# Kernel tuning notes

Measured on AMD Instinct MI355X. Metric: run time of the kernel, lower is better.

The kernel has to match this reference:

```python
import jax, jax.numpy as jnp
import numpy as np


def setup_inputs() -> dict:
    key = jax.random.key(0)
    ks = jax.random.split(key, 8)
    b, l, d, n = 2, 4096, 1024, 16
    s = 0.02
    return {
        "x": jax.random.normal(ks[0], (b, l, d), dtype=jnp.float32),
        "W1": jax.random.normal(ks[1], (d, d), dtype=jnp.float32) * s,
        "b1": jnp.zeros((d,), dtype=jnp.float32),
        "W2": jax.random.normal(ks[2], (n, d), dtype=jnp.float32) * s,
        "b2": jnp.zeros((n,), dtype=jnp.float32),
        "W3": jax.random.normal(ks[3], (n, d), dtype=jnp.float32) * s,
        "b3": jnp.zeros((n,), dtype=jnp.float32),
        "A": jax.random.normal(ks[4], (d, n), dtype=jnp.float32) * s,
    }


def reference(x, W1, b1, W2, b2, W3, b3, A):
    # Faithful to the torch S6.forward as written:
    #   B = fc2(x); C = fc3(x); delta = softplus(fc1(x))
    #   dB = einsum('bld,bln->bldn', delta, B)
    #   h  = dA * 0 + x[..., None] * dB          (h starts at zeros, no scan)
    #   y  = einsum('bln,bldn->bld', C, h)
    # which collapses exactly to y = x * delta * sum_n(C * B).
    # dA = exp(einsum('bld,dn->bldn', delta, A)) is multiplied by zeros and
    # therefore never influences the output (A is a dead parameter here).
    B = jnp.einsum('bld,nd->bln', x, W2) + b2          # (b, l, n)
    C = jnp.einsum('bld,nd->bln', x, W3) + b3          # (b, l, n)
    delta = jax.nn.softplus(jnp.einsum('bld,ed->ble', x, W1) + b1)  # (b, l, d)
    cb = jnp.sum(C * B, axis=-1)                        # (b, l) = sum_n C*B
    y = x * delta * cb[..., None]                       # (b, l, d)
    return y
```

## Files before the change

### kernel.cpp

```cpp
#include <hip/hip_runtime.h>
#include <hip/hip_bf16.h>
#include <stdint.h>

typedef __attribute__((ext_vector_type(8))) short short8;
typedef __attribute__((ext_vector_type(4))) float f32x4;
typedef __attribute__((ext_vector_type(4))) unsigned short us4;

static __device__ __forceinline__ unsigned short f2bf(float f) {
    __hip_bfloat16 h = __float2bfloat16(f);
    union { __hip_bfloat16 h; unsigned short u; } v; v.h = h;
    return v.u;
}
static __device__ __forceinline__ float bf2f(unsigned short h) {
    union { uint32_t u; float f; } v; v.u = ((uint32_t)h) << 16;
    return v.f;
}

static __device__ __forceinline__ short8 cvt8(float4 a, float4 b) {
    short8 r;
    r[0] = (short)f2bf(a.x); r[1] = (short)f2bf(a.y);
    r[2] = (short)f2bf(a.z); r[3] = (short)f2bf(a.w);
    r[4] = (short)f2bf(b.x); r[5] = (short)f2bf(b.y);
    r[6] = (short)f2bf(b.z); r[7] = (short)f2bf(b.w);
    return r;
}

__global__ __launch_bounds__(256) void cb_fused(
    const float* __restrict__ x,
    const float* __restrict__ W1,
    const float* __restrict__ W2,
    const float* __restrict__ b2,
    const float* __restrict__ W3,
    const float* __restrict__ b3,
    unsigned short* __restrict__ xb,
    unsigned short* __restrict__ w1b,
    float* __restrict__ cbo)
{
    const int bid = blockIdx.x;
    const int t = threadIdx.x;

    if (bid >= 512) {
        const int base = (bid - 512) * 4096 + t;
        const float4* w4 = (const float4*)W1;
#pragma unroll
        for (int i = 0; i < 16; ++i) {
            float4 v = w4[base + i * 256];
            us4 r = { f2bf(v.x), f2bf(v.y), f2bf(v.z), f2bf(v.w) };
            *(us4*)&w1b[(size_t)(base + i * 256) * 4] = r;
        }
        return;
    }

    __shared__ float red[4][2][16][16];

    const int wave = t >> 6, lane = t & 63;
    const int r0 = bid * 16;
    const int rrow = lane & 15;
    const int klane = (lane >> 4) * 8;
    const size_t xrow = (size_t)(r0 + rrow) * 1024;
    const int k0 = wave * 256;

    f32x4 accB = {0.f, 0.f, 0.f, 0.f};
    f32x4 accC = {0.f, 0.f, 0.f, 0.f};

#pragma unroll
    for (int ks = 0; ks < 256; ks += 32) {
        const int k = k0 + ks + klane;
        float4 xa = *(const float4*)&x[xrow + k];
        float4 xc = *(const float4*)&x[xrow + k + 4];
        short8 af = cvt8(xa, xc);
        *(short8*)&xb[xrow + k] = af;
        float4 w2a = *(const float4*)&W2[(size_t)rrow * 1024 + k];
        float4 w2c = *(const float4*)&W2[(size_t)rrow * 1024 + k + 4];
        float4 w3a = *(const float4*)&W3[(size_t)rrow * 1024 + k];
        float4 w3c = *(const float4*)&W3[(size_t)rrow * 1024 + k + 4];
        short8 w2f = cvt8(w2a, w2c);
        short8 w3f = cvt8(w3a, w3c);
        accB = __builtin_amdgcn_mfma_f32_16x16x32_bf16(af, w2f, accB, 0, 0, 0);
        accC = __builtin_amdgcn_mfma_f32_16x16x32_bf16(af, w3f, accC, 0, 0, 0);
    }

#pragma unroll
    for (int j = 0; j < 4; ++j) {
        red[wave][0][(lane >> 4) * 4 + j][lane & 15] = accB[j];
        red[wave][1][(lane >> 4) * 4 + j][lane & 15] = accC[j];
    }
    __syncthreads();

    if (wave == 0) {
        const int n = lane & 15;
        const float b2v = b2[n], b3v = b3[n];
        float prod[4];
#pragma unroll
        for (int j = 0; j < 4; ++j) {
            const int row = (lane >> 4) * 4 + j;
            float Bv = red[0][0][row][n] + red[1][0][row][n]
                     + red[2][0][row][n] + red[3][0][row][n] + b2v;
            float Cv = red[0][1][row][n] + red[1][1][row][n]
                     + red[2][1][row][n] + red[3][1][row][n] + b3v;
            prod[j] = Bv * Cv;
        }
#pragma unroll
        for (int off = 1; off < 16; off <<= 1)
#pragma unroll
            for (int j = 0; j < 4; ++j)
                prod[j] += __shfl_xor(prod[j], off, 64);
        if ((lane & 15) == 0) {
#pragma unroll
            for (int j = 0; j < 4; ++j)
                cbo[r0 + (lane >> 4) * 4 + j] = prod[j];
        }
    }
}

__global__ __launch_bounds__(256, 2) void gemm_kernel(
    const unsigned short* __restrict__ xb,
    const unsigned short* __restrict__ w1b,
    const float* __restrict__ b1,
    const float* __restrict__ cb,
    float* __restrict__ y)
{
    __shared__ unsigned short As[2][128 * 64];
    __shared__ unsigned short Bs[2][128 * 64];

    const int wg = blockIdx.x;
    const int nid = (wg & 7) * 64 + (wg >> 3);
    const int row0 = (nid >> 3) * 128;
    const int col0 = (nid & 7) * 128;

    const int t = threadIdx.x;
    const int wid = t >> 6, lane = t & 63;
    const int wm = wid >> 1, wn = wid & 1;

    const int lrow = lane >> 3;
    const int gslot = (lane & 7) ^ lrow;

    f32x4 acc[4][4];
#pragma unroll
    for (int m = 0; m < 4; ++m)
#pragma unroll
        for (int n = 0; n < 4; ++n)
            acc[m][n] = (f32x4){0.f, 0.f, 0.f, 0.f};

    auto STAGE = [&](int b, int kt) {
#pragma unroll
        for (int p = 0; p < 4; ++p) {
            const int grp = p * 4 + wid;
            const int row = grp * 8 + lrow;
            const int gc = kt + gslot * 8;
            const unsigned short* ga = &xb[(size_t)(row0 + row) * 1024 + gc];
            const unsigned short* gb = &w1b[(size_t)(col0 + row) * 1024 + gc];
            __builtin_amdgcn_global_load_lds(
                (const __attribute__((address_space(1))) void*)ga,
                (__attribute__((address_space(3))) void*)&As[b][grp * 512 + lane * 8], 16, 0, 0);
            __builtin_amdgcn_global_load_lds(
                (const __attribute__((address_space(1))) void*)gb,
                (__attribute__((address_space(3))) void*)&Bs[b][grp * 512 + lane * 8], 16, 0, 0);
        }
    };

    STAGE(0, 0);
    asm volatile("s_waitcnt vmcnt(0)" ::: "memory");
    __builtin_amdgcn_s_barrier();
    __builtin_amdgcn_sched_barrier(0);

    const int ro = lane & 15;
    const int sh = lane >> 4;

    for (int tk = 0; tk < 16; ++tk) {
        const int cur = tk & 1;
        if (tk < 15) {
            STAGE(cur ^ 1, (tk + 1) * 64);
            asm volatile("s_waitcnt vmcnt(8)" ::: "memory");
        } else {
            asm volatile("s_waitcnt vmcnt(0)" ::: "memory");
        }
        __builtin_amdgcn_s_barrier();
        __builtin_amdgcn_sched_barrier(0);

        short8 af[2][4], bfr[2][4];
#pragma unroll
        for (int ks = 0; ks < 2; ++ks) {
            const int s = ks * 4 + sh;
#pragma unroll
            for (int m = 0; m < 4; ++m) {
                const int ar = wm * 64 + m * 16 + ro;
                af[ks][m]  = *(const short8*)&As[cur][ar * 64 + ((s ^ (ro & 7)) << 3)];
                const int br = wn * 64 + m * 16 + ro;
                bfr[ks][m] = *(const short8*)&Bs[cur][br * 64 + ((s ^ (ro & 7)) << 3)];
            }
        }
        __builtin_amdgcn_s_setprio(1);
#pragma unroll
        for (int ks = 0; ks < 2; ++ks)
#pragma unroll
            for (int m = 0; m < 4; ++m)
#pragma unroll
                for (int n = 0; n < 4; ++n)
                    acc[m][n] = __builtin_amdgcn_mfma_f32_16x16x32_bf16(af[ks][m], bfr[ks][n], acc[m][n], 0, 0, 0);
        __builtin_amdgcn_s_setprio(0);

        asm volatile("s_waitcnt lgkmcnt(0)" ::: "memory");
        __builtin_amdgcn_s_barrier();
        __builtin_amdgcn_sched_barrier(0);
    }

#pragma unroll
    for (int m = 0; m < 4; ++m) {
        const int grow_base = row0 + wm * 64 + m * 16 + (lane >> 4) * 4;
#pragma unroll
        for (int n = 0; n < 4; ++n) {
            const int gcol = col0 + wn * 64 + n * 16 + (lane & 15);
            const float bv = b1[gcol];
#pragma unroll
            for (int j = 0; j < 4; ++j) {
                const int grow = grow_base + j;
                const float v = acc[m][n][j] + bv;
                const float sp = (v > 15.f) ? v : __logf(1.f + __expf(v));
                const size_t off = (size_t)grow * 1024 + gcol;
                y[off] = bf2f(xb[off]) * sp * cb[grow];
            }
        }
    }
}

extern "C" void kernel_launch(void* const* d_in, const int* in_sizes, int n_in,
                              void* d_out, int out_size, void* d_ws, size_t ws_size,
                              hipStream_t stream) {
    const float* x  = (const float*)d_in[0];
    const float* W1 = (const float*)d_in[1];
    const float* b1 = (const float*)d_in[2];
    const float* W2 = (const float*)d_in[3];
    const float* b2 = (const float*)d_in[4];
    const float* W3 = (const float*)d_in[5];
    const float* b3 = (const float*)d_in[6];

    float* y = (float*)d_out;

    unsigned short* xb  = (unsigned short*)d_ws;
    unsigned short* w1b = xb + (size_t)8192 * 1024;
    float* cbuf = (float*)(w1b + (size_t)1024 * 1024);

    cb_fused<<<576, 256, 0, stream>>>(x, W1, W2, b2, W3, b3, xb, w1b, cbuf);
    gemm_kernel<<<512, 256, 0, stream>>>(xb, w1b, b1, cbuf, y);
}
```

Before: 46.12 us.

## Split GEMM k-tile staging into halves interleaved with MFMA; widen prologue blocks to 512

The GEMM main loop now issues the next tile's global-to-LDS loads in two halves. The second half is issued between the two k-substeps of MFMA work, and LDS fragment reads are split per substep so loads overlap compute. The first kernel doubles its block size to 512 threads, so each wave covers 128 of K instead of 256 and the reduction runs over 8 waves. This shortens per-wave serial loads in the prologue kernel at the cost of more shared-memory reduction work and a more intricate vmcnt schedule.

```diff
diff --git a/kernel.cpp b/kernel.cpp
--- a/kernel.cpp
+++ b/kernel.cpp
@@ -25,7 +25,7 @@
     return r;
 }
 
-__global__ __launch_bounds__(256) void cb_fused(
+__global__ __launch_bounds__(512) void cb_fused(
     const float* __restrict__ x,
     const float* __restrict__ W1,
     const float* __restrict__ W2,
@@ -43,28 +43,28 @@
         const int base = (bid - 512) * 4096 + t;
         const float4* w4 = (const float4*)W1;
 #pragma unroll
-        for (int i = 0; i < 16; ++i) {
-            float4 v = w4[base + i * 256];
+        for (int i = 0; i < 8; ++i) {
+            float4 v = w4[base + i * 512];
             us4 r = { f2bf(v.x), f2bf(v.y), f2bf(v.z), f2bf(v.w) };
-            *(us4*)&w1b[(size_t)(base + i * 256) * 4] = r;
+            *(us4*)&w1b[(size_t)(base + i * 512) * 4] = r;
         }
         return;
     }
 
-    __shared__ float red[4][2][16][16];
+    __shared__ float red[8][2][16][16];
 
     const int wave = t >> 6, lane = t & 63;
     const int r0 = bid * 16;
     const int rrow = lane & 15;
     const int klane = (lane >> 4) * 8;
     const size_t xrow = (size_t)(r0 + rrow) * 1024;
-    const int k0 = wave * 256;
+    const int k0 = wave * 128;
 
     f32x4 accB = {0.f, 0.f, 0.f, 0.f};
     f32x4 accC = {0.f, 0.f, 0.f, 0.f};
 
 #pragma unroll
-    for (int ks = 0; ks < 256; ks += 32) {
+    for (int ks = 0; ks < 128; ks += 32) {
         const int k = k0 + ks + klane;
         float4 xa = *(const float4*)&x[xrow + k];
         float4 xc = *(const float4*)&x[xrow + k + 4];
@@ -94,10 +94,12 @@
 #pragma unroll
         for (int j = 0; j < 4; ++j) {
             const int row = (lane >> 4) * 4 + j;
-            float Bv = red[0][0][row][n] + red[1][0][row][n]
-                     + red[2][0][row][n] + red[3][0][row][n] + b2v;
-            float Cv = red[0][1][row][n] + red[1][1][row][n]
-                     + red[2][1][row][n] + red[3][1][row][n] + b3v;
+            float Bv = b2v, Cv = b3v;
+#pragma unroll
+            for (int w = 0; w < 8; ++w) {
+                Bv += red[w][0][row][n];
+                Cv += red[w][1][row][n];
+            }
             prod[j] = Bv * Cv;
         }
 #pragma unroll
@@ -142,9 +144,9 @@
         for (int n = 0; n < 4; ++n)
             acc[m][n] = (f32x4){0.f, 0.f, 0.f, 0.f};
 
-    auto STAGE = [&](int b, int kt) {
-#pragma unroll
-        for (int p = 0; p < 4; ++p) {
+    auto STAGE_HALF = [&](int b, int kt, int h) {
+#pragma unroll
+        for (int p = 2 * h; p < 2 * h + 2; ++p) {
             const int grp = p * 4 + wid;
             const int row = grp * 8 + lrow;
             const int gc = kt + gslot * 8;
@@ -159,48 +161,62 @@
         }
     };
 
-    STAGE(0, 0);
-    asm volatile("s_waitcnt vmcnt(0)" ::: "memory");
-    __builtin_amdgcn_s_barrier();
-    __builtin_amdgcn_sched_barrier(0);
+    STAGE_HALF(0, 0, 0);
+    STAGE_HALF(0, 0, 1);
 
     const int ro = lane & 15;
     const int sh = lane >> 4;
 
     for (int tk = 0; tk < 16; ++tk) {
         const int cur = tk & 1;
+
         if (tk < 15) {
-            STAGE(cur ^ 1, (tk + 1) * 64);
-            asm volatile("s_waitcnt vmcnt(8)" ::: "memory");
+            STAGE_HALF(cur ^ 1, (tk + 1) * 64, 0);
+            asm volatile("s_waitcnt vmcnt(4)" ::: "memory");
         } else {
             asm volatile("s_waitcnt vmcnt(0)" ::: "memory");
         }
         __builtin_amdgcn_s_barrier();
         __builtin_amdgcn_sched_barrier(0);
 
-        short8 af[2][4], bfr[2][4];
-#pragma unroll
-        for (int ks = 0; ks < 2; ++ks) {
-            const int s = ks * 4 + sh;
+        short8 af[4], bfr[4];
+        {
+            const int s = (sh ^ (ro & 7)) << 3;
 #pragma unroll
             for (int m = 0; m < 4; ++m) {
-                const int ar = wm * 64 + m * 16 + ro;
-                af[ks][m]  = *(const short8*)&As[cur][ar * 64 + ((s ^ (ro & 7)) << 3)];
-                const int br = wn * 64 + m * 16 + ro;
-                bfr[ks][m] = *(const short8*)&Bs[cur][br * 64 + ((s ^ (ro & 7)) << 3)];
-            }
-        }
+                af[m]  = *(const short8*)&As[cur][(wm * 64 + m * 16 + ro) * 64 + s];
+                bfr[m] = *(const short8*)&Bs[cur][(wn * 64 + m * 16 + ro) * 64 + s];
+            }
+        }
+        asm volatile("s_waitcnt lgkmcnt(0)" ::: "memory");
+        __builtin_amdgcn_sched_barrier(0);
         __builtin_amdgcn_s_setprio(1);
 #pragma unroll
-        for (int ks = 0; ks < 2; ++ks)
-#pragma unroll
-            for (int m = 0; m < 4; ++m)
-#pragma unroll
-                for (int n = 0; n < 4; ++n)
-                    acc[m][n] = __builtin_amdgcn_mfma_f32_16x16x32_bf16(af[ks][m], bfr[ks][n], acc[m][n], 0, 0, 0);
+        for (int m = 0; m < 4; ++m)
+#pragma unroll
+            for (int n = 0; n < 4; ++n)
+                acc[m][n] = __builtin_amdgcn_mfma_f32_16x16x32_bf16(af[m], bfr[n], acc[m][n], 0, 0, 0);
         __builtin_amdgcn_s_setprio(0);
 
+        if (tk < 15) STAGE_HALF(cur ^ 1, (tk + 1) * 64, 1);
+        {
+            const int s = ((4 + sh) ^ (ro & 7)) << 3;
+#pragma unroll
+            for (int m = 0; m < 4; ++m) {
+                af[m]  = *(const short8*)&As[cur][(wm * 64 + m * 16 + ro) * 64 + s];
+                bfr[m] = *(const short8*)&Bs[cur][(wn * 64 + m * 16 + ro) * 64 + s];
+            }
+        }
         asm volatile("s_waitcnt lgkmcnt(0)" ::: "memory");
+        __builtin_amdgcn_sched_barrier(0);
+        __builtin_amdgcn_s_setprio(1);
+#pragma unroll
+        for (int m = 0; m < 4; ++m)
+#pragma unroll
+            for (int n = 0; n < 4; ++n)
+                acc[m][n] = __builtin_amdgcn_mfma_f32_16x16x32_bf16(af[m], bfr[n], acc[m][n], 0, 0, 0);
+        __builtin_amdgcn_s_setprio(0);
+
         __builtin_amdgcn_s_barrier();
         __builtin_amdgcn_sched_barrier(0);
     }
@@ -241,6 +257,6 @@
     unsigned short* w1b = xb + (size_t)8192 * 1024;
     float* cbuf = (float*)(w1b + (size_t)1024 * 1024);
 
-    cb_fused<<<576, 256, 0, stream>>>(x, W1, W2, b2, W3, b3, xb, w1b, cbuf);
+    cb_fused<<<576, 512, 0, stream>>>(x, W1, W2, b2, W3, b3, xb, w1b, cbuf);
     gemm_kernel<<<512, 256, 0, stream>>>(xb, w1b, b1, cbuf, y);
 }
```

After: 50.76 us. 1.1x slower.

## Shrink GEMM tile to 128x64 with K-step 32 for more workgroups

Applied to the files above, without the earlier changes.

Changes the main GEMM tile from 128x128 with K-step 64 to 128x64 with K-step 32. This doubles the grid to 1024 workgroups and raises the occupancy hint to 4 blocks per CU. The LDS staging is rewritten with a new XOR swizzle for 32-wide rows, and the block-to-tile mapping is adjusted to match. The aim is better CU fill and latency hiding on a grid of only 512 blocks. In exchange, arithmetic intensity per tile drops, operand loads from global and L2 double, and each of the twice-as-many K iterations does fewer MFMAs per barrier.

```diff
diff --git a/kernel.cpp b/kernel.cpp
--- a/kernel.cpp
+++ b/kernel.cpp
@@ -113,49 +113,50 @@
     }
 }
 
-__global__ __launch_bounds__(256, 2) void gemm_kernel(
+__global__ __launch_bounds__(256, 4) void gemm_kernel(
     const unsigned short* __restrict__ xb,
     const unsigned short* __restrict__ w1b,
     const float* __restrict__ b1,
     const float* __restrict__ cb,
     float* __restrict__ y)
 {
-    __shared__ unsigned short As[2][128 * 64];
-    __shared__ unsigned short Bs[2][128 * 64];
+    __shared__ unsigned short As[2][128 * 32];
+    __shared__ unsigned short Bs[2][64 * 32];
 
     const int wg = blockIdx.x;
-    const int nid = (wg & 7) * 64 + (wg >> 3);
-    const int row0 = (nid >> 3) * 128;
-    const int col0 = (nid & 7) * 128;
+    const int nid = (wg & 7) * 128 + (wg >> 3);
+    const int row0 = (nid >> 4) * 128;
+    const int col0 = (nid & 15) * 64;
 
     const int t = threadIdx.x;
     const int wid = t >> 6, lane = t & 63;
     const int wm = wid >> 1, wn = wid & 1;
 
-    const int lrow = lane >> 3;
-    const int gslot = (lane & 7) ^ lrow;
-
-    f32x4 acc[4][4];
+    f32x4 acc[4][2];
 #pragma unroll
     for (int m = 0; m < 4; ++m)
 #pragma unroll
-        for (int n = 0; n < 4; ++n)
+        for (int n = 0; n < 2; ++n)
             acc[m][n] = (f32x4){0.f, 0.f, 0.f, 0.f};
 
+    const int rg = t >> 2, sl = t & 3;
     auto STAGE = [&](int b, int kt) {
 #pragma unroll
-        for (int p = 0; p < 4; ++p) {
-            const int grp = p * 4 + wid;
-            const int row = grp * 8 + lrow;
-            const int gc = kt + gslot * 8;
+        for (int p = 0; p < 2; ++p) {
+            const int row = rg + p * 64;
+            const int gc = kt + ((sl ^ ((row >> 1) & 3)) << 3);
             const unsigned short* ga = &xb[(size_t)(row0 + row) * 1024 + gc];
+            __builtin_amdgcn_global_load_lds(
+                (const __attribute__((address_space(1))) void*)ga,
+                (__attribute__((address_space(3))) void*)&As[b][row * 32 + sl * 8], 16, 0, 0);
+        }
+        {
+            const int row = rg;
+            const int gc = kt + ((sl ^ ((row >> 1) & 3)) << 3);
             const unsigned short* gb = &w1b[(size_t)(col0 + row) * 1024 + gc];
             __builtin_amdgcn_global_load_lds(
-                (const __attribute__((address_space(1))) void*)ga,
-                (__attribute__((address_space(3))) void*)&As[b][grp * 512 + lane * 8], 16, 0, 0);
-            __builtin_amdgcn_global_load_lds(
                 (const __attribute__((address_space(1))) void*)gb,
-                (__attribute__((address_space(3))) void*)&Bs[b][grp * 512 + lane * 8], 16, 0, 0);
+                (__attribute__((address_space(3))) void*)&Bs[b][row * 32 + sl * 8], 16, 0, 0);
         }
     };
 
@@ -167,37 +168,32 @@
     const int ro = lane & 15;
     const int sh = lane >> 4;
 
-    for (int tk = 0; tk < 16; ++tk) {
+    for (int tk = 0; tk < 32; ++tk) {
         const int cur = tk & 1;
-        if (tk < 15) {
-            STAGE(cur ^ 1, (tk + 1) * 64);
-            asm volatile("s_waitcnt vmcnt(8)" ::: "memory");
+        if (tk < 31) {
+            STAGE(cur ^ 1, (tk + 1) * 32);
+            asm volatile("s_waitcnt vmcnt(3)" ::: "memory");
         } else {
             asm volatile("s_waitcnt vmcnt(0)" ::: "memory");
         }
         __builtin_amdgcn_s_barrier();
         __builtin_amdgcn_sched_barrier(0);
 
-        short8 af[2][4], bfr[2][4];
-#pragma unroll
-        for (int ks = 0; ks < 2; ++ks) {
-            const int s = ks * 4 + sh;
-#pragma unroll
-            for (int m = 0; m < 4; ++m) {
-                const int ar = wm * 64 + m * 16 + ro;
-                af[ks][m]  = *(const short8*)&As[cur][ar * 64 + ((s ^ (ro & 7)) << 3)];
-                const int br = wn * 64 + m * 16 + ro;
-                bfr[ks][m] = *(const short8*)&Bs[cur][br * 64 + ((s ^ (ro & 7)) << 3)];
-            }
-        }
+        short8 af[4], bfr[2];
+        const int s = (sh ^ ((ro >> 1) & 3)) << 3;
+#pragma unroll
+        for (int m = 0; m < 4; ++m)
+            af[m]  = *(const short8*)&As[cur][(wm * 64 + m * 16 + ro) * 32 + s];
+#pragma unroll
+        for (int n = 0; n < 2; ++n)
+            bfr[n] = *(const short8*)&Bs[cur][(wn * 32 + n * 16 + ro) * 32 + s];
+
         __builtin_amdgcn_s_setprio(1);
 #pragma unroll
-        for (int ks = 0; ks < 2; ++ks)
-#pragma unroll
-            for (int m = 0; m < 4; ++m)
-#pragma unroll
-                for (int n = 0; n < 4; ++n)
-                    acc[m][n] = __builtin_amdgcn_mfma_f32_16x16x32_bf16(af[ks][m], bfr[ks][n], acc[m][n], 0, 0, 0);
+        for (int m = 0; m < 4; ++m)
+#pragma unroll
+            for (int n = 0; n < 2; ++n)
+                acc[m][n] = __builtin_amdgcn_mfma_f32_16x16x32_bf16(af[m], bfr[n], acc[m][n], 0, 0, 0);
         __builtin_amdgcn_s_setprio(0);
 
         asm volatile("s_waitcnt lgkmcnt(0)" ::: "memory");
@@ -209,8 +205,8 @@
     for (int m = 0; m < 4; ++m) {
         const int grow_base = row0 + wm * 64 + m * 16 + (lane >> 4) * 4;
 #pragma unroll
-        for (int n = 0; n < 4; ++n) {
-            const int gcol = col0 + wn * 64 + n * 16 + (lane & 15);
+        for (int n = 0; n < 2; ++n) {
+            const int gcol = col0 + wn * 32 + n * 16 + (lane & 15);
             const float bv = b1[gcol];
 #pragma unroll
             for (int j = 0; j < 4; ++j) {
@@ -242,5 +238,5 @@
     float* cbuf = (float*)(w1b + (size_t)1024 * 1024);
 
     cb_fused<<<576, 256, 0, stream>>>(x, W1, W2, b2, W3, b3, xb, w1b, cbuf);
-    gemm_kernel<<<512, 256, 0, stream>>>(xb, w1b, b1, cbuf, y);
-}
+    gemm_kernel<<<1024, 256, 0, stream>>>(xb, w1b, b1, cbuf, y);
+}
```

Measured after the change: 51.06 us. +10.7%, slower.
